# Optimization experiments

Measured on AMD Instinct MI355X. Metric: run time of the kernel, lower is better.

## Reference

```python
import jax, jax.numpy as jnp
import numpy as np
from jax import lax

NUM_CLASSES = 4   # includes ignore label 0
IGNORE = 0
MAX_SAMPLES = 1024
HALF = MAX_SAMPLES // 2
BIG = 1 << 30     # sentinel key for invalid/unselected pixels


def setup_inputs() -> dict:
    key = jax.random.key(0)
    k1, k2, k3 = jax.random.split(key, 3)
    B, C, H, W = 4, 64, 256, 256
    feat_map = jax.random.normal(k1, (B, C, H, W), dtype=jnp.float32)
    labels = jax.random.randint(k2, (B, H, W), 0, NUM_CLASSES, dtype=jnp.int32)
    preds = jax.random.normal(k3, (B, NUM_CLASSES, H, W), dtype=jnp.float32)
    return {"feat_map": feat_map, "labels": labels, "preds": preds}


def _soft_dilate2d(x):
    # F.max_pool2d(x, kernel=3, stride=1, padding=1) on [B,1,H,W]
    return lax.reduce_window(x, -jnp.inf, lax.max, (1, 1, 3, 3), (1, 1, 1, 1), "SAME")


def _per_pair(fm, lab, pd, cls):
    # fm: [C, N] features, lab: [N] int labels, pd: [N] dilated pred class, cls: scalar int
    N = lab.shape[0]
    ar = jnp.arange(N)
    clsf = cls.astype(pd.dtype)
    in_cls = lab == cls
    hard = (pd != clsf) & in_cls   # mispredicted (after dilation) pixels of this class
    easy = (pd == clsf) & in_cls
    # torch code uses randperm; reference uses the deterministic identity
    # permutation: keep the first HALF hard pixels (in raster order).
    hard_key = jnp.where(hard, ar, BIG)
    hard_top = jnp.sort(hard_key)[:HALF]                      # [HALF]
    valid_h = (hard_top < BIG).astype(fm.dtype)
    feat_h = fm[:, jnp.where(hard_top < BIG, hard_top, 0)] * valid_h  # [C, HALF], zero-padded
    # rest pool = leftover hard pixels (rank >= HALF) first, then easy pixels;
    # keep first HALF of that concatenation.
    hard_rank = jnp.cumsum(hard) - 1
    easy_rank = jnp.cumsum(easy) - 1
    excess = jnp.maximum(jnp.sum(hard) - HALF, 0)
    rest_key = jnp.where(hard & (hard_rank >= HALF), hard_rank - HALF,
                         jnp.where(easy, excess + easy_rank, BIG))
    order = jnp.argsort(rest_key)[:HALF]                      # pixel indices, valid first
    valid_r = (jnp.take(rest_key, order) < BIG).astype(fm.dtype)
    feat_r = fm[:, order] * valid_r                           # [C, HALF], zero-padded
    return jnp.concatenate([feat_h, feat_r], axis=1)          # [C, MAX_SAMPLES]


def reference(feat_map, labels, preds):
    B, C, H, W = feat_map.shape
    N = H * W
    # softmax preserves argmax -> skip the softmax
    pred_lab = jnp.argmax(preds, axis=1).astype(feat_map.dtype)[:, None]  # [B,1,H,W]
    preds_d = _soft_dilate2d(pred_lab).reshape(B, N)
    feat_flat = feat_map.reshape(B, C, N)
    lab_flat = labels.reshape(B, N)
    # assume all non-ignore classes present in each image (true w.h.p. for
    # random labels over 65536 pixels) -> static total_classes = B*(NUM_CLASSES-1)
    b_idx = jnp.repeat(jnp.arange(B), NUM_CLASSES - 1)
    cls_idx = jnp.tile(jnp.arange(1, NUM_CLASSES), B)
    feat_extract = jax.vmap(_per_pair)(feat_flat[b_idx], lab_flat[b_idx],
                                       preds_d[b_idx], cls_idx)  # [B*(NC-1), C, 1024]
    feat_label = cls_idx.astype(jnp.float32)
    return feat_extract, feat_label
```

## Files before the change

### kernel.cpp

```cpp
#include <hip/hip_runtime.h>

#define BB 4
#define CC 64
#define HH 256
#define WW 256
#define NPIX (HH*WW)
#define NCLS 4
#define NPAIR 12
#define HALF 512
#define MAXS 1024
#define NOUT (NPAIR*CC*MAXS)
#define CHUNK 4096
#define NCHUNK (NPIX/CHUNK)
#define NBAND 64
#define BANDPIX (NPIX/NBAND)

__global__ void __launch_bounds__(256) k_dargmax(
        const float* __restrict__ preds, const int* __restrict__ labels,
        unsigned char* __restrict__ pd, unsigned* __restrict__ bandCounts) {
    __shared__ unsigned char vm[4][WW];
    __shared__ unsigned wsum[4][3];
    int bx = blockIdx.x;
    int b = bx >> 6, band = bx & 63;
    int y0 = band * 4;
    int x = threadIdx.x;
    const float* pb = preds + (size_t)b * NCLS * NPIX;

    unsigned char am[6];
#pragma unroll
    for (int r = 0; r < 6; ++r) {
        int y = y0 + r - 1;
        unsigned char a = 0;
        if (y >= 0 && y < HH) {
            const float* p = pb + y * WW + x;
            float best = p[0];
            int arg = 0;
#pragma unroll
            for (int c = 1; c < NCLS; ++c) {
                float v = p[(size_t)c * NPIX];
                if (v > best) { best = v; arg = c; }
            }
            a = (unsigned char)arg;
        }
        am[r] = a;
    }
    unsigned char vmr[4];
#pragma unroll
    for (int ry = 0; ry < 4; ++ry) {
        int m = am[ry];
        if (am[ry + 1] > m) m = am[ry + 1];
        if (am[ry + 2] > m) m = am[ry + 2];
        vmr[ry] = (unsigned char)m;
        vm[ry][x] = (unsigned char)m;
    }
    __syncthreads();

    unsigned pk[3] = {0u, 0u, 0u};
#pragma unroll
    for (int ry = 0; ry < 4; ++ry) {
        int m = vmr[ry];
        if (x > 0)      { int v = vm[ry][x - 1]; if (v > m) m = v; }
        if (x < WW - 1) { int v = vm[ry][x + 1]; if (v > m) m = v; }
        int idx = b * NPIX + (y0 + ry) * WW + x;
        pd[idx] = (unsigned char)m;
        int l = labels[idx];
#pragma unroll
        for (int c = 0; c < 3; ++c)
            if (l == c + 1) pk[c] += (m == c + 1) ? (1u << 16) : 1u;
    }
    int lane = x & 63, w = x >> 6;
#pragma unroll
    for (int c = 0; c < 3; ++c)
#pragma unroll
        for (int off = 32; off > 0; off >>= 1)
            pk[c] += (unsigned)__shfl_down((int)pk[c], off, 64);
    if (lane == 0) { wsum[w][0] = pk[0]; wsum[w][1] = pk[1]; wsum[w][2] = pk[2]; }
    __syncthreads();
    if (x < 3)
        bandCounts[(b * 3 + x) * NBAND + band] =
            wsum[0][x] + wsum[1][x] + wsum[2][x] + wsum[3][x];
}

__global__ void __launch_bounds__(256) k_assign(
        const int* __restrict__ labels, const unsigned char* __restrict__ pd,
        const unsigned* __restrict__ bandCounts, unsigned* __restrict__ pairTotals,
        int* __restrict__ slots, float* __restrict__ out) {
    int pair = blockIdx.x >> 4, chunk = blockIdx.x & 15;
    int b = pair / 3, cls = pair % 3 + 1;
    int t = threadIdx.x;
    __shared__ unsigned bc[NBAND];
    __shared__ unsigned ws[4];
    if (t < NBAND) bc[t] = bandCounts[pair * NBAND + t];
    __syncthreads();
    unsigned base = 0, total = 0;
    int cut = chunk * 4;
#pragma unroll
    for (int i = 0; i < NBAND; ++i) {
        unsigned v = bc[i];
        total += v;
        if (i < cut) base += v;
    }
    if (chunk == 0 && t == 0) {
        pairTotals[pair] = total;
        out[NOUT + pair] = (float)cls;
    }
    int excess = (int)(total & 0xffffu) - HALF;
    if (excess < 0) excess = 0;
    int baseH = (int)(base & 0xffffu), baseE = (int)(base >> 16);
    if (baseH >= MAXS && HALF + excess + baseE >= MAXS) return;

    const int4* lab4 = (const int4*)(labels + b * NPIX + chunk * CHUNK + t * 16);
    const uint4* pd16 = (const uint4*)(pd + b * NPIX + chunk * CHUNK + t * 16);
    int4 l0 = lab4[0], l1 = lab4[1], l2 = lab4[2], l3 = lab4[3];
    uint4 dp = pd16[0];
    int ls[16] = {l0.x, l0.y, l0.z, l0.w, l1.x, l1.y, l1.z, l1.w,
                  l2.x, l2.y, l2.z, l2.w, l3.x, l3.y, l3.z, l3.w};
    unsigned char ds[16];
    unsigned dw[4] = {dp.x, dp.y, dp.z, dp.w};
#pragma unroll
    for (int j = 0; j < 16; ++j) ds[j] = (dw[j >> 2] >> ((j & 3) * 8)) & 0xff;

    unsigned mine = 0;
#pragma unroll
    for (int j = 0; j < 16; ++j)
        if (ls[j] == cls) mine += (ds[j] == cls) ? (1u << 16) : 1u;

    int lane = t & 63, w = t >> 6;
    unsigned v = mine;
#pragma unroll
    for (int off = 1; off < 64; off <<= 1) {
        unsigned u = (unsigned)__shfl_up((int)v, off, 64);
        if (lane >= off) v += u;
    }
    if (lane == 63) ws[w] = v;
    __syncthreads();
    unsigned waveBase = 0;
    for (int i = 0; i < w; ++i) waveBase += ws[i];
    unsigned excl = waveBase + v - mine;

    int hr = baseH + (int)(excl & 0xffffu);
    int er = baseE + (int)(excl >> 16);
    int pixBase = chunk * CHUNK + t * 16;
    int* sl = slots + pair * MAXS;
#pragma unroll
    for (int j = 0; j < 16; ++j) {
        if (ls[j] == cls) {
            if (ds[j] != cls) {
                if (hr < MAXS) sl[hr] = pixBase + j;
                hr++;
            } else {
                int pos = HALF + excess + er;
                if (pos < MAXS) sl[pos] = pixBase + j;
                er++;
            }
        }
    }
}

__global__ void __launch_bounds__(256) k_gather(
        const float* __restrict__ feat, const int* __restrict__ slots,
        const unsigned* __restrict__ pairTotals, float* __restrict__ out) {
    int i = blockIdx.x * 256 + threadIdx.x;
    int q = i << 2;
    int pair = q >> 16;
    unsigned tot = pairTotals[pair];
    int Nh = (int)(tot & 0xffffu), Ne = (int)(tot >> 16);
    int excess = Nh - HALF; if (excess < 0) excess = 0;
    int hardEnd = Nh < MAXS ? Nh : MAXS;
    int easyStart = HALF + excess;
    int easyEnd = easyStart + Ne; if (easyEnd > MAXS) easyEnd = MAXS;

    int c = (q >> 10) & (CC - 1);
    int slot = q & (MAXS - 1);
    int b = pair / 3;
    const float* fp = feat + ((size_t)(b * CC + c)) * NPIX;
    const int* sp = slots + pair * MAXS + slot;
    float o[4];
#pragma unroll
    for (int j = 0; j < 4; ++j) {
        int s = slot + j;
        bool valid = (s < hardEnd) || (s >= easyStart && s < easyEnd);
        float val = 0.0f;
        if (valid) val = fp[sp[j]];
        o[j] = val;
    }
    ((float4*)out)[i] = make_float4(o[0], o[1], o[2], o[3]);
}

extern "C" void kernel_launch(void* const* d_in, const int* in_sizes, int n_in,
                              void* d_out, int out_size, void* d_ws, size_t ws_size,
                              hipStream_t stream) {
    const float* feat   = (const float*)d_in[0];
    const int*   labels = (const int*)d_in[1];
    const float* preds  = (const float*)d_in[2];
    float* out = (float*)d_out;

    unsigned char* pd = (unsigned char*)d_ws;
    int* slots = (int*)(pd + BB * NPIX);
    unsigned* bandCounts = (unsigned*)(slots + NPAIR * MAXS);
    unsigned* pairTotals = bandCounts + NPAIR * NBAND;

    k_dargmax<<<NBAND * BB, 256, 0, stream>>>(preds, labels, pd, bandCounts);
    k_assign<<<NPAIR * NCHUNK, 256, 0, stream>>>(labels, pd, bandCounts, pairTotals, slots, out);
    k_gather<<<NOUT / 4 / 256, 256, 0, stream>>>(feat, slots, pairTotals, out);
}
```

Measured before the change: 106.5 us.

## Fuse slot assignment and feature gather into one kernel using shared-memory slots

Merges the assign and gather kernels. Each block now recomputes its pair's slot list by scanning all chunks serially into shared memory, then gathers four channels of features. This drops one kernel launch and the global slots/pairTotals round trip. In exchange, each pair's scan is repeated in 16 blocks, and the gather runs on only 192 blocks, so it has less parallelism to hide latency on its random loads.

```diff
diff --git a/kernel.cpp b/kernel.cpp
--- a/kernel.cpp
+++ b/kernel.cpp
@@ -13,7 +13,7 @@
 #define CHUNK 4096
 #define NCHUNK (NPIX/CHUNK)
 #define NBAND 64
-#define BANDPIX (NPIX/NBAND)
+#define CPG 4
 
 __global__ void __launch_bounds__(256) k_dargmax(
         const float* __restrict__ preds, const int* __restrict__ labels,
@@ -81,110 +81,100 @@
             wsum[0][x] + wsum[1][x] + wsum[2][x] + wsum[3][x];
 }
 
-__global__ void __launch_bounds__(256) k_assign(
+__global__ void __launch_bounds__(256) k_asgather(
         const int* __restrict__ labels, const unsigned char* __restrict__ pd,
-        const unsigned* __restrict__ bandCounts, unsigned* __restrict__ pairTotals,
-        int* __restrict__ slots, float* __restrict__ out) {
-    int pair = blockIdx.x >> 4, chunk = blockIdx.x & 15;
+        const unsigned* __restrict__ bandCounts, const float* __restrict__ feat,
+        float* __restrict__ out) {
+    int pair = blockIdx.x >> 4, oc = blockIdx.x & 15;
     int b = pair / 3, cls = pair % 3 + 1;
     int t = threadIdx.x;
-    __shared__ unsigned bc[NBAND];
+    int lane = t & 63, w = t >> 6;
+
+    __shared__ int sl[MAXS];
+    __shared__ unsigned bcs[NBAND];
     __shared__ unsigned ws[4];
-    if (t < NBAND) bc[t] = bandCounts[pair * NBAND + t];
+#pragma unroll
+    for (int j = 0; j < 4; ++j) sl[t + j * 256] = -1;
+    if (t < NBAND) bcs[t] = bandCounts[pair * NBAND + t];
     __syncthreads();
-    unsigned base = 0, total = 0;
-    int cut = chunk * 4;
+
+    unsigned total = 0;
 #pragma unroll
-    for (int i = 0; i < NBAND; ++i) {
-        unsigned v = bc[i];
-        total += v;
-        if (i < cut) base += v;
-    }
-    if (chunk == 0 && t == 0) {
-        pairTotals[pair] = total;
-        out[NOUT + pair] = (float)cls;
-    }
+    for (int i = 0; i < NBAND; ++i) total += bcs[i];
     int excess = (int)(total & 0xffffu) - HALF;
     if (excess < 0) excess = 0;
-    int baseH = (int)(base & 0xffffu), baseE = (int)(base >> 16);
-    if (baseH >= MAXS && HALF + excess + baseE >= MAXS) return;
+    if (oc == 0 && t == 0) out[NOUT + pair] = (float)cls;
 
-    const int4* lab4 = (const int4*)(labels + b * NPIX + chunk * CHUNK + t * 16);
-    const uint4* pd16 = (const uint4*)(pd + b * NPIX + chunk * CHUNK + t * 16);
-    int4 l0 = lab4[0], l1 = lab4[1], l2 = lab4[2], l3 = lab4[3];
-    uint4 dp = pd16[0];
-    int ls[16] = {l0.x, l0.y, l0.z, l0.w, l1.x, l1.y, l1.z, l1.w,
-                  l2.x, l2.y, l2.z, l2.w, l3.x, l3.y, l3.z, l3.w};
-    unsigned char ds[16];
-    unsigned dw[4] = {dp.x, dp.y, dp.z, dp.w};
+    unsigned runBase = 0;
 #pragma unroll
-    for (int j = 0; j < 16; ++j) ds[j] = (dw[j >> 2] >> ((j & 3) * 8)) & 0xff;
+    for (int ch = 0; ch < NCHUNK; ++ch) {
+        unsigned myBase = runBase;
+        runBase += bcs[4 * ch] + bcs[4 * ch + 1] + bcs[4 * ch + 2] + bcs[4 * ch + 3];
+        int baseH = (int)(myBase & 0xffffu), baseE = (int)(myBase >> 16);
+        if (baseH >= MAXS && HALF + excess + baseE >= MAXS) continue;
 
-    unsigned mine = 0;
+        const int4* lab4 = (const int4*)(labels + b * NPIX + ch * CHUNK + t * 16);
+        const uint4* pd16 = (const uint4*)(pd + b * NPIX + ch * CHUNK + t * 16);
+        int4 l0 = lab4[0], l1 = lab4[1], l2 = lab4[2], l3 = lab4[3];
+        uint4 dp = pd16[0];
+        int ls[16] = {l0.x, l0.y, l0.z, l0.w, l1.x, l1.y, l1.z, l1.w,
+                      l2.x, l2.y, l2.z, l2.w, l3.x, l3.y, l3.z, l3.w};
+        unsigned char ds[16];
+        unsigned dw[4] = {dp.x, dp.y, dp.z, dp.w};
 #pragma unroll
-    for (int j = 0; j < 16; ++j)
-        if (ls[j] == cls) mine += (ds[j] == cls) ? (1u << 16) : 1u;
+        for (int j = 0; j < 16; ++j) ds[j] = (dw[j >> 2] >> ((j & 3) * 8)) & 0xff;
 
-    int lane = t & 63, w = t >> 6;
-    unsigned v = mine;
+        unsigned mine = 0;
 #pragma unroll
-    for (int off = 1; off < 64; off <<= 1) {
-        unsigned u = (unsigned)__shfl_up((int)v, off, 64);
-        if (lane >= off) v += u;
-    }
-    if (lane == 63) ws[w] = v;
-    __syncthreads();
-    unsigned waveBase = 0;
-    for (int i = 0; i < w; ++i) waveBase += ws[i];
-    unsigned excl = waveBase + v - mine;
+        for (int j = 0; j < 16; ++j)
+            if (ls[j] == cls) mine += (ds[j] == cls) ? (1u << 16) : 1u;
 
-    int hr = baseH + (int)(excl & 0xffffu);
-    int er = baseE + (int)(excl >> 16);
-    int pixBase = chunk * CHUNK + t * 16;
-    int* sl = slots + pair * MAXS;
+        unsigned v = mine;
 #pragma unroll
-    for (int j = 0; j < 16; ++j) {
-        if (ls[j] == cls) {
-            if (ds[j] != cls) {
-                if (hr < MAXS) sl[hr] = pixBase + j;
-                hr++;
-            } else {
-                int pos = HALF + excess + er;
-                if (pos < MAXS) sl[pos] = pixBase + j;
-                er++;
+        for (int off = 1; off < 64; off <<= 1) {
+            unsigned u = (unsigned)__shfl_up((int)v, off, 64);
+            if (lane >= off) v += u;
+        }
+        if (lane == 63) ws[w] = v;
+        __syncthreads();
+        unsigned waveBase = 0;
+        for (int i = 0; i < w; ++i) waveBase += ws[i];
+        unsigned excl = waveBase + v - mine;
+
+        int hr = baseH + (int)(excl & 0xffffu);
+        int er = baseE + (int)(excl >> 16);
+        int pixBase = ch * CHUNK + t * 16;
+#pragma unroll
+        for (int j = 0; j < 16; ++j) {
+            if (ls[j] == cls) {
+                if (ds[j] != cls) {
+                    if (hr < MAXS) sl[hr] = pixBase + j;
+                    hr++;
+                } else {
+                    int pos = HALF + excess + er;
+                    if (pos < MAXS) sl[pos] = pixBase + j;
+                    er++;
+                }
             }
         }
+        __syncthreads();
     }
-}
+    __syncthreads();
 
-__global__ void __launch_bounds__(256) k_gather(
-        const float* __restrict__ feat, const int* __restrict__ slots,
-        const unsigned* __restrict__ pairTotals, float* __restrict__ out) {
-    int i = blockIdx.x * 256 + threadIdx.x;
-    int q = i << 2;
-    int pair = q >> 16;
-    unsigned tot = pairTotals[pair];
-    int Nh = (int)(tot & 0xffffu), Ne = (int)(tot >> 16);
-    int excess = Nh - HALF; if (excess < 0) excess = 0;
-    int hardEnd = Nh < MAXS ? Nh : MAXS;
-    int easyStart = HALF + excess;
-    int easyEnd = easyStart + Ne; if (easyEnd > MAXS) easyEnd = MAXS;
-
-    int c = (q >> 10) & (CC - 1);
-    int slot = q & (MAXS - 1);
-    int b = pair / 3;
-    const float* fp = feat + ((size_t)(b * CC + c)) * NPIX;
-    const int* sp = slots + pair * MAXS + slot;
-    float o[4];
+    int slot = t * 4;
+    int p0 = sl[slot], p1 = sl[slot + 1], p2 = sl[slot + 2], p3 = sl[slot + 3];
+    const float* fb = feat + ((size_t)(b * CC + oc * CPG)) * NPIX;
+    float* ob = out + (size_t)pair * CC * MAXS + (size_t)(oc * CPG) * MAXS + slot;
 #pragma unroll
-    for (int j = 0; j < 4; ++j) {
-        int s = slot + j;
-        bool valid = (s < hardEnd) || (s >= easyStart && s < easyEnd);
-        float val = 0.0f;
-        if (valid) val = fp[sp[j]];
-        o[j] = val;
+    for (int c = 0; c < CPG; ++c) {
+        const float* fp = fb + (size_t)c * NPIX;
+        float4 o;
+        o.x = (p0 >= 0) ? fp[p0] : 0.0f;
+        o.y = (p1 >= 0) ? fp[p1] : 0.0f;
+        o.z = (p2 >= 0) ? fp[p2] : 0.0f;
+        o.w = (p3 >= 0) ? fp[p3] : 0.0f;
+        *(float4*)(ob + c * MAXS) = o;
     }
-    ((float4*)out)[i] = make_float4(o[0], o[1], o[2], o[3]);
 }
 
 extern "C" void kernel_launch(void* const* d_in, const int* in_sizes, int n_in,
@@ -196,11 +186,8 @@
     float* out = (float*)d_out;
 
     unsigned char* pd = (unsigned char*)d_ws;
-    int* slots = (int*)(pd + BB * NPIX);
-    unsigned* bandCounts = (unsigned*)(slots + NPAIR * MAXS);
-    unsigned* pairTotals = bandCounts + NPAIR * NBAND;
+    unsigned* bandCounts = (unsigned*)(pd + BB * NPIX);
 
     k_dargmax<<<NBAND * BB, 256, 0, stream>>>(preds, labels, pd, bandCounts);
-    k_assign<<<NPAIR * NCHUNK, 256, 0, stream>>>(labels, pd, bandCounts, pairTotals, slots, out);
-    k_gather<<<NOUT / 4 / 256, 256, 0, stream>>>(feat, slots, pairTotals, out);
+    k_asgather<<<NPAIR * NCHUNK, 256, 0, stream>>>(labels, pd, bandCounts, feat, out);
 }
```

Measured after the change: 136.5 us. 1.28x slower.
